# Kernel optimization log

Hardware: AMD Instinct MI355X
Metric: run time of the kernel (lower is better)

Reference implementation:

```python
import jax, jax.numpy as jnp
import numpy as np

PATCH = 4   # patch_size
TOPK = 2    # top_k

B, H, W, C = 4, 128, 128, 256
FF, E = 1024, 4


def setup_inputs() -> dict:
    key = jax.random.key(0)
    k1, k2, k3, k4 = jax.random.split(key, 4)
    x = jax.random.normal(k1, (B, H, W, C), dtype=jnp.float32)
    Wg = jax.random.normal(k2, (E, C), dtype=jnp.float32) * 0.01   # router gate (std=0.01 init)
    lim1 = (6.0 / (C + FF)) ** 0.5                                  # xavier_uniform bounds
    W1 = jax.random.uniform(k3, (E, FF, C), minval=-lim1, maxval=lim1, dtype=jnp.float32)
    b1 = jnp.zeros((E, FF), dtype=jnp.float32)
    W2 = jax.random.uniform(k4, (E, C, FF), minval=-lim1, maxval=lim1, dtype=jnp.float32)
    b2 = jnp.zeros((E, C), dtype=jnp.float32)
    return {"x": x, "Wg": Wg, "W1": W1, "b1": b1, "W2": W2, "b2": b2}


def reference(x, Wg, W1, b1, W2, b2):
    Bs, Hs, Ws, Cs = x.shape
    Es = Wg.shape[0]
    ph = pw = PATCH
    nh, nw = Hs // ph, Ws // pw
    P = nh * nw
    # [B, nh, ph, nw, pw, C]
    xp = x.reshape(Bs, nh, ph, nw, pw, Cs)
    # --- router: per-patch avg pool + linear gate ---
    means = xp.mean(axis=(2, 4))                                  # [B, nh, nw, C]
    logits = jnp.einsum('bhwc,ec->bhwe', means, Wg).reshape(Bs, P, Es)
    probs = jax.nn.softmax(logits, axis=-1)
    w, idx = jax.lax.top_k(probs, TOPK)                           # [B, P, K]
    w = w / (w.sum(axis=-1, keepdims=True) + 1e-9)
    # dense combine weights per expert: [B, P, E]
    comb = (jax.nn.one_hot(idx, Es, dtype=w.dtype) * w[..., None]).sum(axis=-2)
    # --- expert dispatch/combine over patch tokens ---
    tokens = xp.transpose(0, 1, 3, 2, 4, 5).reshape(Bs, P, ph * pw, Cs)  # [B,P,T,C]
    out = jnp.zeros_like(tokens)
    for e in range(Es):  # small fixed expert set
        h = jax.nn.gelu(jnp.einsum('bptc,fc->bptf', tokens, W1[e]) + b1[e],
                        approximate=False)
        y = jnp.einsum('bptf,cf->bptc', h, W2[e]) + b2[e]
        out = out + comb[:, :, e, None, None] * y
    # reassemble patches -> [B, H, W, C]
    out = out.reshape(Bs, nh, nw, ph, pw, Cs).transpose(0, 1, 3, 2, 4, 5)
    return out.reshape(Bs, Hs, Ws, Cs)
```

## Files before the change

kernel.cpp:

```cpp
#include <hip/hip_runtime.h>
#include <hip/hip_bf16.h>
#include <cstdint>

#define NB 4
#define NH 128
#define NW 128
#define NC 256
#define NFF 1024
#define NE 4
#define NPATCH 4096
#define NPAIR 16
#define PPB 4
#define BM 64
#define FFC 128
#define NCHUNK_TOT 16

typedef __attribute__((ext_vector_type(8))) short short8;
typedef __attribute__((ext_vector_type(8))) unsigned short ushort8;
typedef __attribute__((ext_vector_type(16))) float f32x16;

__device__ __forceinline__ unsigned short f2b(float f) {
  union { float f; uint32_t u; } v; v.f = f;
  uint32_t u = v.u + 0x7FFFu + ((v.u >> 16) & 1u);
  return (unsigned short)(u >> 16);
}

__device__ __forceinline__ float gelu_f(float v) {
  float u = v * v;
  float t = __builtin_fmaf(u, 0.044715f, 1.0f) * v;
  float e = __builtin_amdgcn_exp2f(t * -2.3022083f);
  return v * __builtin_amdgcn_rcpf(1.0f + e);
}

__device__ __forceinline__ void bar_lgkm() {
  asm volatile("s_waitcnt lgkmcnt(0)" ::: "memory");
  __builtin_amdgcn_s_barrier();
}

__global__ __launch_bounds__(256) void convert_kernel(
    const float* __restrict__ W1, const float* __restrict__ W2,
    unsigned short* __restrict__ W1b, unsigned short* __restrict__ W2b,
    int* __restrict__ cnt, int n) {
  int i = blockIdx.x * blockDim.x + threadIdx.x;
  if (i < NPAIR) cnt[i] = 0;
  if (i < n) {
    W1b[i] = f2b(W1[i]);
    W2b[i] = f2b(W2[i]);
  }
}

__global__ __launch_bounds__(256) void router_kernel(
    const float* __restrict__ x, const float* __restrict__ Wg,
    int* __restrict__ cnt, int* __restrict__ plist, float2* __restrict__ wlist) {
  int p = blockIdx.x;
  int b = p >> 10, pi = p & 1023;
  int phi = pi >> 5, pwi = pi & 31;
  int c = threadIdx.x;

  const float* base = x + (((size_t)(b * NH + phi * 4) * NW) + pwi * 4) * NC + c;
  float s = 0.f;
#pragma unroll
  for (int i = 0; i < 4; i++)
#pragma unroll
    for (int j = 0; j < 4; j++)
      s += base[(i * NW + j) * NC];
  float mean = s * (1.f / 16.f);

  __shared__ float m_lds[NC];
  __shared__ double logit_lds[NE];
  m_lds[c] = mean;
  __syncthreads();

  int wid = c >> 6, lane = c & 63;
  {
    const float* wg = Wg + wid * NC;
    double acc = 0.0;
#pragma unroll
    for (int q = 0; q < 4; q++)
      acc += (double)m_lds[lane + q * 64] * (double)wg[lane + q * 64];
    for (int off = 32; off; off >>= 1) acc += __shfl_down(acc, off);
    if (lane == 0) logit_lds[wid] = acc;
  }
  __syncthreads();

  if (c == 0) {
    double l[NE], pp[NE];
    double mx = -1e300;
#pragma unroll
    for (int i = 0; i < NE; i++) { l[i] = logit_lds[i]; mx = fmax(mx, l[i]); }
    double sum = 0.0;
#pragma unroll
    for (int i = 0; i < NE; i++) { pp[i] = exp(l[i] - mx); sum += pp[i]; }
#pragma unroll
    for (int i = 0; i < NE; i++) pp[i] /= sum;
    int i1 = 0; double p1 = pp[0];
    for (int i = 1; i < NE; i++) if (pp[i] > p1) { p1 = pp[i]; i1 = i; }
    int i2 = -1; double p2 = -1.0;
    for (int i = 0; i < NE; i++) {
      if (i == i1) continue;
      if (pp[i] > p2) { p2 = pp[i]; i2 = i; }
    }
    double den = p1 + p2 + 1e-9;
    float w1 = (float)(p1 / den), w2 = (float)(p2 / den);
    int pr = i1 * NE + i2;
    int pos = atomicAdd(&cnt[pr], 1);
    plist[pr * NPATCH + pos] = p;
    wlist[pr * NPATCH + pos] = make_float2(w1, w2);
  }
}

__global__ __launch_bounds__(64) void worklist_kernel(
    const int* __restrict__ cnt, int* __restrict__ wl) {
  int lane = threadIdx.x;
  int cA[8], cB[8], mx = 0;
#pragma unroll
  for (int xc = 0; xc < 8; ++xc) {
    cA[xc] = (cnt[xc] + PPB - 1) / PPB;
    cB[xc] = (cnt[xc + 8] + PPB - 1) / PPB;
    int t = cA[xc] + cB[xc];
    mx = (t > mx) ? t : mx;
  }
  if (lane == 0) wl[0] = 8 * mx;
  int x = lane & 7, sub = lane >> 3;
  int nA = cA[x], tot = cA[x] + cB[x];
  for (int r = sub; r < mx; r += 8) {
    int ent = -1;
    if (r < nA) ent = (x << 12) | (r * PPB);
    else if (r < tot) ent = ((x + 8) << 12) | ((r - nA) * PPB);
    wl[1 + x + 8 * r] = ent;
  }
}

__global__ __launch_bounds__(256, 3) void ffn_kernel(
    const float* __restrict__ x, const float* __restrict__ b1,
    const float* __restrict__ b2, const unsigned short* __restrict__ W1b,
    const unsigned short* __restrict__ W2b, const int* __restrict__ cnt,
    const int* __restrict__ plist, const float2* __restrict__ wlist,
    const int* __restrict__ wl, float* __restrict__ out) {
  __shared__ unsigned short Xf[2 * 16 * 512];
  __shared__ unsigned short Hf[2 * 8 * 512];

  int slotb = blockIdx.x;
  if (slotb >= wl[0]) return;
  int ent = wl[1 + slotb];
  if (ent < 0) return;
  int pr = ent >> 12, pbase = ent & 4095;
  int e1 = pr >> 2, e2 = pr & 3;
  int n = cnt[pr];

  int tid = threadIdx.x, lane = tid & 63, wid = tid >> 6;
  int l31 = lane & 31, lh = lane >> 5;

  const int*    pl  = plist + pr * NPATCH + pbase;
  const float2* wlp = wlist + pr * NPATCH + pbase;

  float wvA[PPB], wvB[PPB];
#pragma unroll
  for (int q = 0; q < PPB; q++) {
    if (pbase + q < n) { float2 w = wlp[q]; wvA[q] = w.x; wvB[q] = w.y; }
    else { wvA[q] = 0.f; wvB[q] = 0.f; }
  }

  {
    int r  = tid >> 2;
    int c0 = (tid & 3) * 64;
    int pid = (pbase + (r >> 4) < n) ? pl[r >> 4] : -1;
    int t = r & 15;
    int tt = r >> 5, t32 = r & 31;
    if (pid >= 0) {
      int b = pid >> 10, pi = pid & 1023;
      int phi = pi >> 5, pwi = pi & 31;
      const float* src =
          x + (((size_t)(b * NH + phi * 4 + (t >> 2)) * NW) + pwi * 4 + (t & 3)) * NC + c0;
#pragma unroll
      for (int kb = 0; kb < 8; kb++) {
        float4 v0 = *reinterpret_cast<const float4*>(src + kb * 8);
        float4 v1 = *reinterpret_cast<const float4*>(src + kb * 8 + 4);
        ushort8 h;
        h[0] = f2b(v0.x); h[1] = f2b(v0.y); h[2] = f2b(v0.z); h[3] = f2b(v0.w);
        h[4] = f2b(v1.x); h[5] = f2b(v1.y); h[6] = f2b(v1.z); h[7] = f2b(v1.w);
        int k = c0 + kb * 8;
        int uidx = (tt * 16 + (k >> 4)) * 512 + (((k >> 3) & 1) * 32 + t32) * 8;
        *reinterpret_cast<ushort8*>(&Xf[uidx]) = h;
      }
    } else {
      ushort8 h = (ushort8)0;
#pragma unroll
      for (int kb = 0; kb < 8; kb++) {
        int k = c0 + kb * 8;
        int uidx = (tt * 16 + (k >> 4)) * 512 + (((k >> 3) & 1) * 32 + t32) * 8;
        *reinterpret_cast<ushort8*>(&Xf[uidx]) = h;
      }
    }
  }
  bar_lgkm();

  const unsigned short* W1A = W1b + (size_t)e1 * NFF * NC;
  const unsigned short* W1B = W1b + (size_t)e2 * NFF * NC;
  const unsigned short* W2A = W2b + (size_t)e1 * NC * NFF;
  const unsigned short* W2B = W2b + (size_t)e2 * NC * NFF;
  const float* b1A = b1 + e1 * NFF;
  const float* b1B = b1 + e2 * NFF;

  int wf = wid;
  int wc = wid;

  f32x16 y00 = (f32x16)0.f, y01 = (f32x16)0.f;
  f32x16 y10 = (f32x16)0.f, y11 = (f32x16)0.f;
  f32x16 a0, a1;
  ushort4 hreg[8];

#pragma unroll 1
  for (int j = 0; j < NCHUNK_TOT; ++j) {
    int fc = j & 7;
    const unsigned short* W1e = (j < 8) ? W1A : W1B;
    const float* b1e = (j < 8) ? b1A : b1B;
    a0 = (f32x16)0.f; a1 = (f32x16)0.f;

    const unsigned short* wrow = W1e + (size_t)(fc * FFC + wf * 32 + l31) * NC + lh * 8;
#pragma unroll
    for (int kf = 0; kf < 16; ++kf) {
      short8 aW = *reinterpret_cast<const short8*>(wrow + kf * 16);
      short8 bX0 = *reinterpret_cast<const short8*>(&Xf[(0 * 16 + kf) * 512 + lane * 8]);
      short8 bX1 = *reinterpret_cast<const short8*>(&Xf[(1 * 16 + kf) * 512 + lane * 8]);
      a0 = __builtin_amdgcn_mfma_f32_32x32x16_bf16(aW, bX0, a0, 0, 0, 0);
      a1 = __builtin_amdgcn_mfma_f32_32x32x16_bf16(aW, bX1, a1, 0, 0, 0);
    }

#pragma unroll
    for (int tt = 0; tt < 2; ++tt) {
      const f32x16& A = (tt == 0) ? a0 : a1;
      float wlo = (j < 8) ? wvA[tt * 2]     : wvB[tt * 2];
      float whi = (j < 8) ? wvA[tt * 2 + 1] : wvB[tt * 2 + 1];
      float w = (l31 >= 16) ? whi : wlo;
#pragma unroll
      for (int q = 0; q < 4; ++q) {
        int qs = q * 8 + lh * 4;
        float4 bv = *reinterpret_cast<const float4*>(b1e + fc * FFC + wf * 32 + qs);
        ushort4 hp;
        hp.x = f2b(gelu_f(A[q * 4 + 0] + bv.x) * w);
        hp.y = f2b(gelu_f(A[q * 4 + 1] + bv.y) * w);
        hp.z = f2b(gelu_f(A[q * 4 + 2] + bv.z) * w);
        hp.w = f2b(gelu_f(A[q * 4 + 3] + bv.w) * w);
        hreg[tt * 4 + q] = hp;
      }
    }

    bar_lgkm();
#pragma unroll
    for (int tt = 0; tt < 2; ++tt) {
#pragma unroll
      for (int q = 0; q < 4; ++q) {
        int qs = q * 8 + lh * 4;
        int page = tt * 8 + wf * 2 + (qs >> 4);
        int uidx = page * 512 + (((qs >> 3) & 1) * 32 + l31) * 8 + (qs & 4);
        *reinterpret_cast<ushort4*>(&Hf[uidx]) = hreg[tt * 4 + q];
      }
    }
    bar_lgkm();

    const unsigned short* W2e = (j < 8) ? W2A : W2B;
    const unsigned short* w0 = W2e + (size_t)(wc * 64 + l31) * NFF + fc * FFC + lh * 8;
    const unsigned short* w1 = W2e + (size_t)(wc * 64 + 32 + l31) * NFF + fc * FFC + lh * 8;
#pragma unroll
    for (int kkf = 0; kkf < 8; ++kkf) {
      short8 aH0 = *reinterpret_cast<const short8*>(&Hf[(0 * 8 + kkf) * 512 + lane * 8]);
      short8 aH1 = *reinterpret_cast<const short8*>(&Hf[(1 * 8 + kkf) * 512 + lane * 8]);
      short8 bW0 = *reinterpret_cast<const short8*>(w0 + kkf * 16);
      short8 bW1 = *reinterpret_cast<const short8*>(w1 + kkf * 16);
      y00 = __builtin_amdgcn_mfma_f32_32x32x16_bf16(aH0, bW0, y00, 0, 0, 0);
      y01 = __builtin_amdgcn_mfma_f32_32x32x16_bf16(aH1, bW0, y01, 0, 0, 0);
      y10 = __builtin_amdgcn_mfma_f32_32x32x16_bf16(aH0, bW1, y10, 0, 0, 0);
      y11 = __builtin_amdgcn_mfma_f32_32x32x16_bf16(aH1, bW1, y11, 0, 0, 0);
    }
  }

#pragma unroll
  for (int ct = 0; ct < 2; ++ct) {
    int cc = wc * 64 + ct * 32 + l31;
    float bA = b2[e1 * NC + cc];
    float bB = b2[e2 * NC + cc];
#pragma unroll
    for (int tt = 0; tt < 2; ++tt) {
      const f32x16& Y = (ct == 0) ? ((tt == 0) ? y00 : y01)
                                  : ((tt == 0) ? y10 : y11);
#pragma unroll
      for (int q = 0; q < 4; ++q) {
        int pslot = tt * 2 + (q >> 1);
        if (pbase + pslot >= n) continue;
        int pid = pl[pslot];
        float wA = wvA[pslot], wB = wvB[pslot];
        int b = pid >> 10, pi = pid & 1023;
        int phi = pi >> 5, pwi = pi & 31;
        float bias = wA * bA + wB * bB;
#pragma unroll
        for (int i = 0; i < 4; ++i) {
          int tok = 8 * (q & 1) + 4 * lh + i;
          float* dst =
              out + (((size_t)(b * NH + phi * 4 + (tok >> 2)) * NW) + pwi * 4 + (tok & 3)) * NC;
          dst[cc] = Y[q * 4 + i] + bias;
        }
      }
    }
  }
}

extern "C" void kernel_launch(void* const* d_in, const int* in_sizes, int n_in,
                              void* d_out, int out_size, void* d_ws, size_t ws_size,
                              hipStream_t stream) {
  const float* x  = (const float*)d_in[0];
  const float* Wg = (const float*)d_in[1];
  const float* W1 = (const float*)d_in[2];
  const float* b1 = (const float*)d_in[3];
  const float* W2 = (const float*)d_in[4];
  const float* b2 = (const float*)d_in[5];
  float* out = (float*)d_out;

  char* ws = (char*)d_ws;
  unsigned short* W1b = (unsigned short*)ws;
  unsigned short* W2b = (unsigned short*)(ws + (size_t)2 * 1024 * 1024);
  int*    cnt   = (int*)(ws + (size_t)4 * 1024 * 1024);
  int*    plist = (int*)(ws + (size_t)4 * 1024 * 1024 + 256);
  float2* wlist = (float2*)(ws + (size_t)4 * 1024 * 1024 + 256 +
                            (size_t)NPAIR * NPATCH * sizeof(int));
  int*    wl    = (int*)(ws + (size_t)5 * 1024 * 1024);

  convert_kernel<<<dim3(4096), dim3(256), 0, stream>>>(W1, W2, W1b, W2b, cnt, NE * NFF * NC);
  router_kernel<<<dim3(NPATCH), dim3(256), 0, stream>>>(x, Wg, cnt, plist, wlist);
  worklist_kernel<<<dim3(1), dim3(64), 0, stream>>>(cnt, wl);

  ffn_kernel<<<dim3(8200), dim3(256), 0, stream>>>(
      x, b1, b2, W1b, W2b, cnt, plist, wlist, wl, out);
}
```

Measured before the change: 439.0 us.

## Split fused expert FFN into separate GEMM1 and GEMM2 kernels via global H buffer

The fused per-block FFN, which alternated W1 GEMM+GELU and W2 GEMM through shared memory with barriers, becomes two kernels. The first writes bf16 hidden activations to a workspace buffer and the second reads them back to do the down projection, run in one to four groups depending on workspace size. Later groups accumulate into the output. The worklist is also compacted into a contiguous prefix sum over expert pairs, so padding slots are gone and the grid shrinks. This removes intra-loop barriers and lets each phase run with its own occupancy, at the cost of extra global traffic for H (up to hundreds of MB), extra launches, and read-modify-write of the output when more than one group runs.

```diff
diff --git a/kernel.cpp b/kernel.cpp
--- a/kernel.cpp
+++ b/kernel.cpp
@@ -13,7 +13,7 @@
 #define PPB 4
 #define BM 64
 #define FFC 128
-#define NCHUNK_TOT 16
+#define NSLOT 1040
 
 typedef __attribute__((ext_vector_type(8))) short short8;
 typedef __attribute__((ext_vector_type(8))) unsigned short ushort8;
@@ -112,38 +112,31 @@
 __global__ __launch_bounds__(64) void worklist_kernel(
     const int* __restrict__ cnt, int* __restrict__ wl) {
   int lane = threadIdx.x;
-  int cA[8], cB[8], mx = 0;
-#pragma unroll
-  for (int xc = 0; xc < 8; ++xc) {
-    cA[xc] = (cnt[xc] + PPB - 1) / PPB;
-    cB[xc] = (cnt[xc + 8] + PPB - 1) / PPB;
-    int t = cA[xc] + cB[xc];
-    mx = (t > mx) ? t : mx;
-  }
-  if (lane == 0) wl[0] = 8 * mx;
-  int x = lane & 7, sub = lane >> 3;
-  int nA = cA[x], tot = cA[x] + cB[x];
-  for (int r = sub; r < mx; r += 8) {
-    int ent = -1;
-    if (r < nA) ent = (x << 12) | (r * PPB);
-    else if (r < tot) ent = ((x + 8) << 12) | ((r - nA) * PPB);
-    wl[1 + x + 8 * r] = ent;
-  }
-}
-
-__global__ __launch_bounds__(256, 3) void ffn_kernel(
+  if (lane < NPAIR) {
+    int base = 0, mynb = 0;
+    for (int q = 0; q < NPAIR; ++q) {
+      int nb = (cnt[q] + PPB - 1) / PPB;
+      if (q < lane) base += nb;
+      if (q == lane) mynb = nb;
+    }
+    for (int i = 0; i < mynb; ++i)
+      wl[1 + base + i] = (lane << 12) | (i * PPB);
+    if (lane == NPAIR - 1) wl[0] = base + mynb;
+  }
+}
+
+
+__global__ __launch_bounds__(256, 3) void g1_kernel(
     const float* __restrict__ x, const float* __restrict__ b1,
-    const float* __restrict__ b2, const unsigned short* __restrict__ W1b,
-    const unsigned short* __restrict__ W2b, const int* __restrict__ cnt,
+    const unsigned short* __restrict__ W1b, const int* __restrict__ cnt,
     const int* __restrict__ plist, const float2* __restrict__ wlist,
-    const int* __restrict__ wl, float* __restrict__ out) {
+    const int* __restrict__ wl, unsigned short* __restrict__ Hbuf,
+    int group, int cpg) {
   __shared__ unsigned short Xf[2 * 16 * 512];
-  __shared__ unsigned short Hf[2 * 8 * 512];
-
-  int slotb = blockIdx.x;
-  if (slotb >= wl[0]) return;
-  int ent = wl[1 + slotb];
-  if (ent < 0) return;
+
+  int s = blockIdx.x;
+  if (s >= wl[0]) return;
+  int ent = wl[1 + s];
   int pr = ent >> 12, pbase = ent & 4095;
   int e1 = pr >> 2, e2 = pr & 3;
   int n = cnt[pr];
@@ -195,77 +188,93 @@
   }
   bar_lgkm();
 
-  const unsigned short* W1A = W1b + (size_t)e1 * NFF * NC;
-  const unsigned short* W1B = W1b + (size_t)e2 * NFF * NC;
-  const unsigned short* W2A = W2b + (size_t)e1 * NC * NFF;
-  const unsigned short* W2B = W2b + (size_t)e2 * NC * NFF;
-  const float* b1A = b1 + e1 * NFF;
-  const float* b1B = b1 + e2 * NFF;
-
-  int wf = wid;
+  for (int c = wid; c < cpg; c += 4) {
+    int gc = group * cpg + c;
+    int side = gc >> 3;
+    int fc = gc & 7;
+    const unsigned short* W1e = W1b + (size_t)(side ? e2 : e1) * NFF * NC;
+    const float* b1e = b1 + (side ? e2 : e1) * NFF;
+    char* Hc = (char*)Hbuf + ((size_t)s * cpg + c) * 16384;
+
+    for (int fs = 0; fs < 4; ++fs) {
+      f32x16 a0 = (f32x16)0.f, a1 = (f32x16)0.f;
+      const unsigned short* wrow =
+          W1e + (size_t)(fc * FFC + fs * 32 + l31) * NC + lh * 8;
+#pragma unroll
+      for (int kf = 0; kf < 16; ++kf) {
+        short8 aW = *reinterpret_cast<const short8*>(wrow + kf * 16);
+        short8 bX0 = *reinterpret_cast<const short8*>(&Xf[(0 * 16 + kf) * 512 + lane * 8]);
+        short8 bX1 = *reinterpret_cast<const short8*>(&Xf[(1 * 16 + kf) * 512 + lane * 8]);
+        a0 = __builtin_amdgcn_mfma_f32_32x32x16_bf16(aW, bX0, a0, 0, 0, 0);
+        a1 = __builtin_amdgcn_mfma_f32_32x32x16_bf16(aW, bX1, a1, 0, 0, 0);
+      }
+
+#pragma unroll
+      for (int tt = 0; tt < 2; ++tt) {
+        const f32x16& A = (tt == 0) ? a0 : a1;
+        float wlo = side ? wvB[tt * 2]     : wvA[tt * 2];
+        float whi = side ? wvB[tt * 2 + 1] : wvA[tt * 2 + 1];
+        float w = (l31 >= 16) ? whi : wlo;
+#pragma unroll
+        for (int q = 0; q < 4; ++q) {
+          int qs = q * 8 + lh * 4;
+          float4 bv = *reinterpret_cast<const float4*>(b1e + fc * FFC + fs * 32 + qs);
+          ushort4 hp;
+          hp.x = f2b(gelu_f(A[q * 4 + 0] + bv.x) * w);
+          hp.y = f2b(gelu_f(A[q * 4 + 1] + bv.y) * w);
+          hp.z = f2b(gelu_f(A[q * 4 + 2] + bv.z) * w);
+          hp.w = f2b(gelu_f(A[q * 4 + 3] + bv.w) * w);
+          int page = tt * 8 + fs * 2 + (qs >> 4);
+          *reinterpret_cast<ushort4*>(
+              Hc + page * 1024 + ((qs >> 3) & 1) * 512 + l31 * 16 + (qs & 4) * 2) = hp;
+        }
+      }
+    }
+  }
+}
+
+__global__ __launch_bounds__(256, 3) void g2_kernel(
+    const float* __restrict__ b2, const unsigned short* __restrict__ W2b,
+    const int* __restrict__ cnt, const int* __restrict__ plist,
+    const float2* __restrict__ wlist, const int* __restrict__ wl,
+    const unsigned short* __restrict__ Hbuf, float* __restrict__ out,
+    int group, int cpg) {
+  int s = blockIdx.x;
+  if (s >= wl[0]) return;
+  int ent = wl[1 + s];
+  int pr = ent >> 12, pbase = ent & 4095;
+  int e1 = pr >> 2, e2 = pr & 3;
+  int n = cnt[pr];
+
+  int tid = threadIdx.x, lane = tid & 63, wid = tid >> 6;
+  int l31 = lane & 31, lh = lane >> 5;
+
+  const int*    pl  = plist + pr * NPATCH + pbase;
+  const float2* wlp = wlist + pr * NPATCH + pbase;
+
+  float wvA[PPB], wvB[PPB];
+#pragma unroll
+  for (int q = 0; q < PPB; q++) {
+    if (pbase + q < n) { float2 w = wlp[q]; wvA[q] = w.x; wvB[q] = w.y; }
+    else { wvA[q] = 0.f; wvB[q] = 0.f; }
+  }
+
   int wc = wid;
-
   f32x16 y00 = (f32x16)0.f, y01 = (f32x16)0.f;
   f32x16 y10 = (f32x16)0.f, y11 = (f32x16)0.f;
-  f32x16 a0, a1;
-  ushort4 hreg[8];
-
-#pragma unroll 1
-  for (int j = 0; j < NCHUNK_TOT; ++j) {
-    int fc = j & 7;
-    const unsigned short* W1e = (j < 8) ? W1A : W1B;
-    const float* b1e = (j < 8) ? b1A : b1B;
-    a0 = (f32x16)0.f; a1 = (f32x16)0.f;
-
-    const unsigned short* wrow = W1e + (size_t)(fc * FFC + wf * 32 + l31) * NC + lh * 8;
-#pragma unroll
-    for (int kf = 0; kf < 16; ++kf) {
-      short8 aW = *reinterpret_cast<const short8*>(wrow + kf * 16);
-      short8 bX0 = *reinterpret_cast<const short8*>(&Xf[(0 * 16 + kf) * 512 + lane * 8]);
-      short8 bX1 = *reinterpret_cast<const short8*>(&Xf[(1 * 16 + kf) * 512 + lane * 8]);
-      a0 = __builtin_amdgcn_mfma_f32_32x32x16_bf16(aW, bX0, a0, 0, 0, 0);
-      a1 = __builtin_amdgcn_mfma_f32_32x32x16_bf16(aW, bX1, a1, 0, 0, 0);
-    }
-
-#pragma unroll
-    for (int tt = 0; tt < 2; ++tt) {
-      const f32x16& A = (tt == 0) ? a0 : a1;
-      float wlo = (j < 8) ? wvA[tt * 2]     : wvB[tt * 2];
-      float whi = (j < 8) ? wvA[tt * 2 + 1] : wvB[tt * 2 + 1];
-      float w = (l31 >= 16) ? whi : wlo;
-#pragma unroll
-      for (int q = 0; q < 4; ++q) {
-        int qs = q * 8 + lh * 4;
-        float4 bv = *reinterpret_cast<const float4*>(b1e + fc * FFC + wf * 32 + qs);
-        ushort4 hp;
-        hp.x = f2b(gelu_f(A[q * 4 + 0] + bv.x) * w);
-        hp.y = f2b(gelu_f(A[q * 4 + 1] + bv.y) * w);
-        hp.z = f2b(gelu_f(A[q * 4 + 2] + bv.z) * w);
-        hp.w = f2b(gelu_f(A[q * 4 + 3] + bv.w) * w);
-        hreg[tt * 4 + q] = hp;
-      }
-    }
-
-    bar_lgkm();
-#pragma unroll
-    for (int tt = 0; tt < 2; ++tt) {
-#pragma unroll
-      for (int q = 0; q < 4; ++q) {
-        int qs = q * 8 + lh * 4;
-        int page = tt * 8 + wf * 2 + (qs >> 4);
-        int uidx = page * 512 + (((qs >> 3) & 1) * 32 + l31) * 8 + (qs & 4);
-        *reinterpret_cast<ushort4*>(&Hf[uidx]) = hreg[tt * 4 + q];
-      }
-    }
-    bar_lgkm();
-
-    const unsigned short* W2e = (j < 8) ? W2A : W2B;
+
+  for (int c = 0; c < cpg; ++c) {
+    int gc = group * cpg + c;
+    int side = gc >> 3;
+    int fc = gc & 7;
+    const unsigned short* W2e = W2b + (size_t)(side ? e2 : e1) * NC * NFF;
+    const char* Hc = (const char*)Hbuf + ((size_t)s * cpg + c) * 16384;
     const unsigned short* w0 = W2e + (size_t)(wc * 64 + l31) * NFF + fc * FFC + lh * 8;
     const unsigned short* w1 = W2e + (size_t)(wc * 64 + 32 + l31) * NFF + fc * FFC + lh * 8;
 #pragma unroll
     for (int kkf = 0; kkf < 8; ++kkf) {
-      short8 aH0 = *reinterpret_cast<const short8*>(&Hf[(0 * 8 + kkf) * 512 + lane * 8]);
-      short8 aH1 = *reinterpret_cast<const short8*>(&Hf[(1 * 8 + kkf) * 512 + lane * 8]);
+      short8 aH0 = *reinterpret_cast<const short8*>(Hc + kkf * 1024 + lane * 16);
+      short8 aH1 = *reinterpret_cast<const short8*>(Hc + 8192 + kkf * 1024 + lane * 16);
       short8 bW0 = *reinterpret_cast<const short8*>(w0 + kkf * 16);
       short8 bW1 = *reinterpret_cast<const short8*>(w1 + kkf * 16);
       y00 = __builtin_amdgcn_mfma_f32_32x32x16_bf16(aH0, bW0, y00, 0, 0, 0);
@@ -298,7 +307,8 @@
           int tok = 8 * (q & 1) + 4 * lh + i;
           float* dst =
               out + (((size_t)(b * NH + phi * 4 + (tok >> 2)) * NW) + pwi * 4 + (tok & 3)) * NC;
-          dst[cc] = Y[q * 4 + i] + bias;
+          if (group == 0) dst[cc] = Y[q * 4 + i] + bias;
+          else            dst[cc] = dst[cc] + Y[q * 4 + i];
         }
       }
     }
@@ -325,10 +335,22 @@
                             (size_t)NPAIR * NPATCH * sizeof(int));
   int*    wl    = (int*)(ws + (size_t)5 * 1024 * 1024);
 
+  size_t hoff = (size_t)5 * 1024 * 1024 + 65536;
+  unsigned short* Hbuf = (unsigned short*)(ws + hoff);
+
+  int ngroups, cpg;
+  if (ws_size >= hoff + (size_t)NSLOT * 16 * 16384)      { ngroups = 1; cpg = 16; }
+  else if (ws_size >= hoff + (size_t)NSLOT * 8 * 16384)  { ngroups = 2; cpg = 8;  }
+  else                                                   { ngroups = 4; cpg = 4;  }
+
   convert_kernel<<<dim3(4096), dim3(256), 0, stream>>>(W1, W2, W1b, W2b, cnt, NE * NFF * NC);
   router_kernel<<<dim3(NPATCH), dim3(256), 0, stream>>>(x, Wg, cnt, plist, wlist);
   worklist_kernel<<<dim3(1), dim3(64), 0, stream>>>(cnt, wl);
 
-  ffn_kernel<<<dim3(8200), dim3(256), 0, stream>>>(
-      x, b1, b2, W1b, W2b, cnt, plist, wlist, wl, out);
-}
+  for (int g = 0; g < ngroups; ++g) {
+    g1_kernel<<<dim3(NSLOT), dim3(256), 0, stream>>>(
+        x, b1, W1b, cnt, plist, wlist, wl, Hbuf, g, cpg);
+    g2_kernel<<<dim3(NSLOT), dim3(256), 0, stream>>>(
+        b2, W2b, cnt, plist, wlist, wl, Hbuf, out, g, cpg);
+  }
+}
```

Measured after the change: 770.5 us. 75.5% more time.
